# Kernel tuning notes

Hardware: AMD Instinct MI355X
Metric: run time of the kernel (lower is better)

The kernel has to match this reference:

```python
import jax, jax.numpy as jnp
import numpy as np

INPUT_SIZE = 128
HIDDEN_SIZE = 128
BATCH = 65536


def _xavier(key, shape):
    fan_out, fan_in = shape
    limit = np.sqrt(6.0 / (fan_in + fan_out)).astype(np.float32)
    return jax.random.uniform(key, shape, jnp.float32, -limit, limit)


def setup_inputs() -> dict:
    key = jax.random.key(0)
    ks = jax.random.split(key, 12)
    inp = {
        "x": jax.random.normal(ks[0], (BATCH, INPUT_SIZE), jnp.float32),
        "h_t": jax.random.normal(ks[1], (BATCH, HIDDEN_SIZE), jnp.float32),
        "c_t": jax.random.normal(ks[2], (BATCH, HIDDEN_SIZE), jnp.float32),
        "W_ii": _xavier(ks[3], (HIDDEN_SIZE, INPUT_SIZE)),
        "W_hi": _xavier(ks[4], (HIDDEN_SIZE, HIDDEN_SIZE)),
        "b_i": jnp.zeros((HIDDEN_SIZE,), jnp.float32),
        "W_if": _xavier(ks[5], (HIDDEN_SIZE, INPUT_SIZE)),
        "W_hf": _xavier(ks[6], (HIDDEN_SIZE, HIDDEN_SIZE)),
        "b_f": jnp.zeros((HIDDEN_SIZE,), jnp.float32),
        "W_ig": _xavier(ks[7], (HIDDEN_SIZE, INPUT_SIZE)),
        "W_hg": _xavier(ks[8], (HIDDEN_SIZE, HIDDEN_SIZE)),
        "b_g": jnp.zeros((HIDDEN_SIZE,), jnp.float32),
        "W_io": _xavier(ks[9], (HIDDEN_SIZE, INPUT_SIZE)),
        "W_ho": _xavier(ks[10], (HIDDEN_SIZE, HIDDEN_SIZE)),
        "b_o": jnp.zeros((HIDDEN_SIZE,), jnp.float32),
    }
    return inp


def reference(x, h_t, c_t, W_ii, W_hi, b_i, W_if, W_hf, b_f, W_ig, W_hg, b_g, W_io, W_ho, b_o):
    # Fuse the 8 small GEMMs into 2 concatenated GEMMs, identical math to
    # per-gate F.linear calls (same weights, just stacked along output dim).
    W_x = jnp.concatenate([W_ii, W_if, W_ig, W_io], axis=0)   # [4H, I]
    W_h = jnp.concatenate([W_hi, W_hf, W_hg, W_ho], axis=0)   # [4H, H]
    b = jnp.concatenate([b_i, b_f, b_g, b_o], axis=0)         # [4H]
    gates = x @ W_x.T + h_t @ W_h.T + b                       # [B, 4H]
    i_a, f_a, g_a, o_a = jnp.split(gates, 4, axis=1)
    i_t = jax.nn.sigmoid(i_a)
    f_t = jax.nn.sigmoid(f_a)
    g_t = jnp.tanh(g_a)
    o_t = jax.nn.sigmoid(o_a)
    c_new = f_t * c_t + i_t * g_t
    h_new = o_t * jnp.tanh(c_new)
    return (h_new, c_new)
```

## Files before the change

### kernel.cpp

```cpp
#include <hip/hip_runtime.h>
#include <hip/hip_bf16.h>


typedef short s16x8 __attribute__((ext_vector_type(8)));
typedef float f32x4 __attribute__((ext_vector_type(4)));

__device__ __forceinline__ short f2bf(float f) {
    __hip_bfloat16 h = __float2bfloat16(f);
    return __builtin_bit_cast(short, h);
}
__device__ __forceinline__ float sigm(float x) { return 1.0f / (1.0f + __expf(-x)); }
__device__ __forceinline__ float tanh_f(float x) { return 1.0f - 2.0f / (1.0f + __expf(2.0f * x)); }

__device__ __forceinline__ void dma16(const float* g, void* lds) {
    __builtin_amdgcn_global_load_lds(
        (const __attribute__((address_space(1))) void*)g,
        (__attribute__((address_space(3))) void*)lds, 16, 0, 0);
}

__global__ __launch_bounds__(256)
void repack_weights(const float* __restrict__ Wii, const float* __restrict__ Whi,
                    const float* __restrict__ Wif, const float* __restrict__ Whf,
                    const float* __restrict__ Wig, const float* __restrict__ Whg,
                    const float* __restrict__ Wio, const float* __restrict__ Who,
                    short* __restrict__ ws)
{
    const int t   = blockIdx.x * 256 + threadIdx.x;
    const int fi  = t >> 6;
    const int l   = t & 63;
    const int ks  = fi & 7;
    const int g   = (fi >> 3) & 3;
    const int jt  = fi >> 5;
    const int j   = jt * 16 + (l & 15);
    const int k   = ks * 32 + (l >> 4) * 8;

    const float* wx = (g == 0) ? Wii : (g == 1) ? Wif : (g == 2) ? Wig : Wio;
    const float* wh = (g == 0) ? Whi : (g == 1) ? Whf : (g == 2) ? Whg : Who;
    const float* src = (k < 128) ? (wx + (size_t)j * 128 + k)
                                 : (wh + (size_t)j * 128 + (k - 128));
    f32x4 a = *(const f32x4*)src;
    f32x4 b = *(const f32x4*)(src + 4);
    s16x8 v;
#pragma unroll
    for (int q = 0; q < 4; ++q) { v[q] = f2bf(a[q]); v[4 + q] = f2bf(b[q]); }
    *(s16x8*)(ws + (size_t)t * 8) = v;
}

__global__ __launch_bounds__(256, 4)
void lstm_cell_kernel(const float* __restrict__ X,
                      const float* __restrict__ H,
                      const float* __restrict__ C,
                      const float* __restrict__ Bi, const float* __restrict__ Bf,
                      const float* __restrict__ Bg, const float* __restrict__ Bo,
                      const short* __restrict__ WS,
                      float* __restrict__ OutH,
                      float* __restrict__ OutC)
{
    __shared__ __align__(16) char sA[32768];

    const int tid = threadIdx.x;
    const int l   = tid & 63;
    const int w   = tid >> 6;
    const int lj  = l & 15;
    const int lq  = l >> 4;
    const int B0  = blockIdx.x * 32;

    {
        const int  ci   = l & 31;
        const float* base = (l >= 32) ? H : X;
#pragma unroll
        for (int r = 0; r < 8; ++r) {
            const int m = w * 8 + r;
            const float* src = base + (size_t)(B0 + m) * 128 + ((ci ^ r) << 2);
            dma16(src, (void*)(sA + m * 1024));
        }
    }

    f32x4 acc[2][2][4];
#pragma unroll
    for (int mt = 0; mt < 2; ++mt)
#pragma unroll
        for (int jn = 0; jn < 2; ++jn)
#pragma unroll
            for (int g = 0; g < 4; ++g)
                acc[mt][jn][g] = (f32x4){0.f, 0.f, 0.f, 0.f};

    const short* wsw = WS + (size_t)w * 64 * 512 + l * 8;

    __syncthreads();

#pragma unroll
    for (int ks = 0; ks < 8; ++ks) {
        s16x8 af[2];
#pragma unroll
        for (int mt = 0; mt < 2; ++mt) {
            const int m  = mt * 16 + lj;
            const int cg = ks * 8 + lq * 2;
            const int p0 = (cg & 32) | ((cg & 31) ^ (m & 7));
            const f32x4 q0 = *(const f32x4*)(sA + m * 1024 + p0 * 16);
            const f32x4 q1 = *(const f32x4*)(sA + m * 1024 + (p0 ^ 1) * 16);
            s16x8 v;
#pragma unroll
            for (int q = 0; q < 4; ++q) { v[q] = f2bf(q0[q]); v[4 + q] = f2bf(q1[q]); }
            af[mt] = v;
        }
#pragma unroll
        for (int jn = 0; jn < 2; ++jn)
#pragma unroll
            for (int g = 0; g < 4; ++g) {
                const s16x8 bf = *(const s16x8*)(wsw + (size_t)(jn * 32 + g * 8 + ks) * 512);
                acc[0][jn][g] = __builtin_amdgcn_mfma_f32_16x16x32_bf16(af[0], bf, acc[0][jn][g], 0, 0, 0);
                acc[1][jn][g] = __builtin_amdgcn_mfma_f32_16x16x32_bf16(af[1], bf, acc[1][jn][g], 0, 0, 0);
            }
    }

#pragma unroll
    for (int jn = 0; jn < 2; ++jn) {
        const int j = w * 32 + jn * 16 + lj;
        const float bi  = Bi[j];
        const float bfv = Bf[j];
        const float bg  = Bg[j];
        const float bo  = Bo[j];
#pragma unroll
        for (int mt = 0; mt < 2; ++mt) {
#pragma unroll
            for (int r = 0; r < 4; ++r) {
                const int b = B0 + mt * 16 + lq * 4 + r;
                const size_t idx = (size_t)b * 128 + j;
                const float ia = acc[mt][jn][0][r] + bi;
                const float fa = acc[mt][jn][1][r] + bfv;
                const float ga = acc[mt][jn][2][r] + bg;
                const float oa = acc[mt][jn][3][r] + bo;
                const float it = sigm(ia);
                const float ft = sigm(fa);
                const float gt = tanh_f(ga);
                const float ot = sigm(oa);
                const float co = C[idx];
                const float cn = ft * co + it * gt;
                const float hn = ot * tanh_f(cn);
                OutH[idx] = hn;
                OutC[idx] = cn;
            }
        }
    }
}

extern "C" void kernel_launch(void* const* d_in, const int* in_sizes, int n_in,
                              void* d_out, int out_size, void* d_ws, size_t ws_size,
                              hipStream_t stream) {
    const float* X   = (const float*)d_in[0];
    const float* H   = (const float*)d_in[1];
    const float* C   = (const float*)d_in[2];
    const float* Wii = (const float*)d_in[3];
    const float* Whi = (const float*)d_in[4];
    const float* Bi  = (const float*)d_in[5];
    const float* Wif = (const float*)d_in[6];
    const float* Whf = (const float*)d_in[7];
    const float* Bf  = (const float*)d_in[8];
    const float* Wig = (const float*)d_in[9];
    const float* Whg = (const float*)d_in[10];
    const float* Bg  = (const float*)d_in[11];
    const float* Wio = (const float*)d_in[12];
    const float* Who = (const float*)d_in[13];
    const float* Bo  = (const float*)d_in[14];

    short* ws = (short*)d_ws;

    hipLaunchKernelGGL(repack_weights, dim3(64), dim3(256), 0, stream,
                       Wii, Whi, Wif, Whf, Wig, Whg, Wio, Who, ws);

    float* OutH = (float*)d_out;
    float* OutC = OutH + (size_t)65536 * 128;

    hipLaunchKernelGGL(lstm_cell_kernel, dim3(2048), dim3(256), 0, stream,
                       X, H, C, Bi, Bf, Bg, Bo, ws, OutH, OutC);
}
```

Before: 226.3 us.

## Make LSTM kernel persistent with register-resident weights and double-buffered LDS tiles

Switches to 256 persistent blocks of 512 threads, each processing 8 batch tiles of 32 rows. Each wave keeps its bf16 weight slice in registers, loaded once, instead of reloading weights from global memory per tile. Activation tiles and the matching C values are double-buffered, with explicit vmcnt waits and barriers so the next tile's DMA overlaps the current tile's MFMA and epilogue. The cost is heavy register pressure from 32 weight vectors per lane, fewer blocks than CUs (256 blocks), and fragile hand-tuned vmcnt counts.

```diff
diff --git a/kernel.cpp b/kernel.cpp
--- a/kernel.cpp
+++ b/kernel.cpp
@@ -46,7 +46,7 @@
     *(s16x8*)(ws + (size_t)t * 8) = v;
 }
 
-__global__ __launch_bounds__(256, 4)
+__global__ __launch_bounds__(512, 2)
 void lstm_cell_kernel(const float* __restrict__ X,
                       const float* __restrict__ H,
                       const float* __restrict__ C,
@@ -56,92 +56,132 @@
                       float* __restrict__ OutH,
                       float* __restrict__ OutC)
 {
-    __shared__ __align__(16) char sA[32768];
+    __shared__ __align__(16) char sA[65536];
 
     const int tid = threadIdx.x;
     const int l   = tid & 63;
     const int w   = tid >> 6;
     const int lj  = l & 15;
     const int lq  = l >> 4;
-    const int B0  = blockIdx.x * 32;
-
+    const int jw  = w * 16 + lj;
+    const int tile0 = blockIdx.x * 8;
+
+    s16x8 wreg[4][8];
     {
-        const int  ci   = l & 31;
-        const float* base = (l >= 32) ? H : X;
-#pragma unroll
-        for (int r = 0; r < 8; ++r) {
-            const int m = w * 8 + r;
-            const float* src = base + (size_t)(B0 + m) * 128 + ((ci ^ r) << 2);
-            dma16(src, (void*)(sA + m * 1024));
-        }
+        const short* wp = WS + (size_t)(w * 4) * 8 * 512 + l * 8;
+#pragma unroll
+        for (int g = 0; g < 4; ++g)
+#pragma unroll
+            for (int ks = 0; ks < 8; ++ks)
+                wreg[g][ks] = *(const s16x8*)(wp + (size_t)(g * 8 + ks) * 512);
     }
-
-    f32x4 acc[2][2][4];
-#pragma unroll
-    for (int mt = 0; mt < 2; ++mt)
-#pragma unroll
-        for (int jn = 0; jn < 2; ++jn)
+    const float bi  = Bi[jw];
+    const float bfv = Bf[jw];
+    const float bg  = Bg[jw];
+    const float bo  = Bo[jw];
+
+    const int   ci    = l & 31;
+    const float* abase = (l >= 32) ? H : X;
+
+    auto STAGE = [&](int t) {
+        const int B0 = (tile0 + t) * 32;
+        char* dst = sA + (t & 1) * 32768;
+#pragma unroll
+        for (int r = 0; r < 4; ++r) {
+            const int m = w * 4 + r;
+            const float* src = abase + (size_t)(B0 + m) * 128 + ((ci ^ (m & 7)) << 2);
+            dma16(src, dst + m * 1024);
+        }
+    };
+
+    float cp[2][8];
+    auto CLOAD = [&](int t, float* c) {
+        const int B0 = (tile0 + t) * 32;
+#pragma unroll
+        for (int mt = 0; mt < 2; ++mt)
+#pragma unroll
+            for (int r = 0; r < 4; ++r)
+                c[mt * 4 + r] = C[(size_t)(B0 + mt * 16 + lq * 4 + r) * 128 + jw];
+    };
+
+    STAGE(0);  CLOAD(0, cp[0]);
+    STAGE(1);  CLOAD(1, cp[1]);
+
+#pragma unroll 2
+    for (int t = 0; t < 8; ++t) {
+        if (t == 0)      asm volatile("s_waitcnt vmcnt(0)" ::: "memory");
+        else if (t == 7) asm volatile("s_waitcnt vmcnt(16)" ::: "memory");
+        else             asm volatile("s_waitcnt vmcnt(28)" ::: "memory");
+        __builtin_amdgcn_sched_barrier(0);
+        __builtin_amdgcn_s_barrier();
+        __builtin_amdgcn_sched_barrier(0);
+
+        const char* sb = sA + (t & 1) * 32768;
+
+        f32x4 acc[2][4];
+#pragma unroll
+        for (int mt = 0; mt < 2; ++mt)
 #pragma unroll
             for (int g = 0; g < 4; ++g)
-                acc[mt][jn][g] = (f32x4){0.f, 0.f, 0.f, 0.f};
-
-    const short* wsw = WS + (size_t)w * 64 * 512 + l * 8;
-
-    __syncthreads();
-
-#pragma unroll
-    for (int ks = 0; ks < 8; ++ks) {
-        s16x8 af[2];
-#pragma unroll
-        for (int mt = 0; mt < 2; ++mt) {
-            const int m  = mt * 16 + lj;
-            const int cg = ks * 8 + lq * 2;
-            const int p0 = (cg & 32) | ((cg & 31) ^ (m & 7));
-            const f32x4 q0 = *(const f32x4*)(sA + m * 1024 + p0 * 16);
-            const f32x4 q1 = *(const f32x4*)(sA + m * 1024 + (p0 ^ 1) * 16);
-            s16x8 v;
-#pragma unroll
-            for (int q = 0; q < 4; ++q) { v[q] = f2bf(q0[q]); v[4 + q] = f2bf(q1[q]); }
-            af[mt] = v;
-        }
-#pragma unroll
-        for (int jn = 0; jn < 2; ++jn)
+                acc[mt][g] = (f32x4){0.f, 0.f, 0.f, 0.f};
+
+#pragma unroll
+        for (int ks = 0; ks < 8; ++ks) {
+            s16x8 af[2];
+#pragma unroll
+            for (int mt = 0; mt < 2; ++mt) {
+                const int m  = mt * 16 + lj;
+                const int cg = ks * 8 + lq * 2;
+                const int p0 = (cg & 32) | ((cg & 31) ^ (m & 7));
+                const f32x4 q0 = *(const f32x4*)(sb + m * 1024 + p0 * 16);
+                const f32x4 q1 = *(const f32x4*)(sb + m * 1024 + (p0 ^ 1) * 16);
+                s16x8 v;
+#pragma unroll
+                for (int q = 0; q < 4; ++q) { v[q] = f2bf(q0[q]); v[4 + q] = f2bf(q1[q]); }
+                af[mt] = v;
+            }
 #pragma unroll
             for (int g = 0; g < 4; ++g) {
-                const s16x8 bf = *(const s16x8*)(wsw + (size_t)(jn * 32 + g * 8 + ks) * 512);
-                acc[0][jn][g] = __builtin_amdgcn_mfma_f32_16x16x32_bf16(af[0], bf, acc[0][jn][g], 0, 0, 0);
-                acc[1][jn][g] = __builtin_amdgcn_mfma_f32_16x16x32_bf16(af[1], bf, acc[1][jn][g], 0, 0, 0);
+                acc[0][g] = __builtin_amdgcn_mfma_f32_16x16x32_bf16(af[0], wreg[g][ks], acc[0][g], 0, 0, 0);
+                acc[1][g] = __builtin_amdgcn_mfma_f32_16x16x32_bf16(af[1], wreg[g][ks], acc[1][g], 0, 0, 0);
             }
-    }
-
-#pragma unroll
-    for (int jn = 0; jn < 2; ++jn) {
-        const int j = w * 32 + jn * 16 + lj;
-        const float bi  = Bi[j];
-        const float bfv = Bf[j];
-        const float bg  = Bg[j];
-        const float bo  = Bo[j];
-#pragma unroll
-        for (int mt = 0; mt < 2; ++mt) {
-#pragma unroll
-            for (int r = 0; r < 4; ++r) {
-                const int b = B0 + mt * 16 + lq * 4 + r;
-                const size_t idx = (size_t)b * 128 + j;
-                const float ia = acc[mt][jn][0][r] + bi;
-                const float fa = acc[mt][jn][1][r] + bfv;
-                const float ga = acc[mt][jn][2][r] + bg;
-                const float oa = acc[mt][jn][3][r] + bo;
-                const float it = sigm(ia);
-                const float ft = sigm(fa);
-                const float gt = tanh_f(ga);
-                const float ot = sigm(oa);
-                const float co = C[idx];
-                const float cn = ft * co + it * gt;
-                const float hn = ot * tanh_f(cn);
-                OutH[idx] = hn;
-                OutC[idx] = cn;
+        }
+
+        __builtin_amdgcn_sched_barrier(0);
+        __builtin_amdgcn_s_barrier();
+        __builtin_amdgcn_sched_barrier(0);
+
+        {
+            const int B0 = (tile0 + t) * 32;
+#pragma unroll
+            for (int mt = 0; mt < 2; ++mt) {
+#pragma unroll
+                for (int r = 0; r < 4; ++r) {
+                    const int b = B0 + mt * 16 + lq * 4 + r;
+                    const size_t idx = (size_t)b * 128 + jw;
+                    const float ia = acc[mt][0][r] + bi;
+                    const float fa = acc[mt][1][r] + bfv;
+                    const float ga = acc[mt][2][r] + bg;
+                    const float oa = acc[mt][3][r] + bo;
+                    const float it = sigm(ia);
+                    const float ft = sigm(fa);
+                    const float gt = tanh_f(ga);
+                    const float ot = sigm(oa);
+                    const float co = cp[t & 1][mt * 4 + r];
+                    const float cn = ft * co + it * gt;
+                    const float hn = ot * tanh_f(cn);
+                    OutH[idx] = hn;
+                    OutC[idx] = cn;
+                }
             }
         }
+
+        __builtin_amdgcn_sched_barrier(0);
+        if (t < 6) {
+            STAGE(t + 2);
+            CLOAD(t + 2, cp[t & 1]);
+        }
+        __builtin_amdgcn_sched_barrier(0);
     }
 }
 
@@ -172,6 +212,6 @@
     float* OutH = (float*)d_out;
     float* OutC = OutH + (size_t)65536 * 128;
 
-    hipLaunchKernelGGL(lstm_cell_kernel, dim3(2048), dim3(256), 0, stream,
+    hipLaunchKernelGGL(lstm_cell_kernel, dim3(256), dim3(512), 0, stream,
                        X, H, C, Bi, Bf, Bg, Bo, ws, OutH, OutC);
 }
```

Measured after the change: 185.0 us. 18.2% less time.
